# Kernel tuning notes

Hardware: AMD Instinct MI355X
Metric: run time of the kernel (lower is better)

The kernel has to match this reference:

```python
import jax, jax.numpy as jnp
import numpy as np

DIM = 1024
HEADS = 16
HEAD_DIM = DIM // HEADS  # 64
WIN = 256
B, N = 4, 4096


def setup_inputs() -> dict:
    key = jax.random.key(0)
    k1, k2, k3 = jax.random.split(key, 3)
    x = jax.random.normal(k1, (B, N, DIM), dtype=jnp.float32)
    # torch nn.Linear weights: [out_features, in_features]
    Wqkv = jax.random.normal(k2, (3 * DIM, DIM), dtype=jnp.float32) * (DIM ** -0.5)
    Wproj = jax.random.normal(k3, (DIM, DIM), dtype=jnp.float32) * (DIM ** -0.5)
    return {"x": x, "Wqkv": Wqkv, "Wproj": Wproj}


def reference(x, Wqkv, Wproj):
    Bs, Ns, C = x.shape
    H, hd, W = HEADS, HEAD_DIM, WIN
    # qkv projection -> [3, B, H, N, hd]
    qkv = (x @ Wqkv.T).reshape(Bs, Ns, 3, H, hd).transpose(2, 0, 3, 1, 4)
    q, k, v = qkv[0], qkv[1], qkv[2]
    q = q * (hd ** -0.5)
    pad = (W - Ns % W) % W
    if pad:
        pw = ((0, 0), (0, 0), (0, pad), (0, 0))
        q = jnp.pad(q, pw)
        k = jnp.pad(k, pw)
        v = jnp.pad(v, pw)
    Np = Ns + pad
    Df = (Np * hd) // W  # flattened feature dim per window row
    q = q.reshape(Bs * H, W, Df)
    k = k.reshape(Bs * H, W, Df)
    v = v.reshape(Bs * H, W, Df)
    attn = jax.nn.softmax(jnp.einsum('bwd,bxd->bwx', q, k), axis=-1)  # [B*H, W, W]
    out = jnp.einsum('bwx,bxd->bwd', attn, v)
    out = out.reshape(Bs, H, Np, hd)[:, :, :Ns, :].transpose(0, 2, 1, 3).reshape(Bs, Ns, C)
    return out @ Wproj.T
```

## Files before the change

### kernel.cpp

```cpp
#include <hip/hip_runtime.h>
#include <hip/hip_bf16.h>
#include <stdint.h>


using u16 = unsigned short;
typedef __attribute__((ext_vector_type(4))) float f32x4;
typedef __attribute__((ext_vector_type(8))) short s16x8;

#define MFMA_BF16(a, b, c) __builtin_amdgcn_mfma_f32_16x16x32_bf16((a), (b), (c), 0, 0, 0)

__device__ __forceinline__ u16 f2bf(float f) {
  union { float f; uint32_t u; } v; v.f = f;
  uint32_t r = v.u + 0x7fffu + ((v.u >> 16) & 1u);
  return (u16)(r >> 16);
}

__device__ __forceinline__ void gld16(const void* g, void* l) {
  auto gp = (const __attribute__((address_space(1))) void*)(uintptr_t)g;
  auto lp = (__attribute__((address_space(3))) void*)(uint32_t)(uintptr_t)l;
  __builtin_amdgcn_global_load_lds(gp, lp, 16, 0, 0);
}

__global__ __launch_bounds__(256) void cvt_bf16(const float* __restrict__ in,
                                                u16* __restrict__ out, int n8) {
  for (int i = blockIdx.x * blockDim.x + threadIdx.x; i < n8;
       i += gridDim.x * blockDim.x) {
    const float4* p = (const float4*)in + (size_t)i * 2;
    float4 a = p[0], b = p[1];
    s16x8 r;
    r[0] = (short)f2bf(a.x); r[1] = (short)f2bf(a.y);
    r[2] = (short)f2bf(a.z); r[3] = (short)f2bf(a.w);
    r[4] = (short)f2bf(b.x); r[5] = (short)f2bf(b.y);
    r[6] = (short)f2bf(b.z); r[7] = (short)f2bf(b.w);
    *(s16x8*)(out + (size_t)i * 8) = r;
  }
}

template <bool QS, bool F32OUT>
__global__ __launch_bounds__(256) void gemm_bt(const u16* __restrict__ A,
                                               const u16* __restrict__ W,
                                               void* __restrict__ C, int N) {
  __shared__ alignas(16) u16 lA[128 * 32];
  __shared__ alignas(16) u16 lB[128 * 32];
  const int tid = threadIdx.x;
  const int wv = tid >> 6, lane = tid & 63;
  const int fr = lane & 15, fg = lane >> 4;
  const int li = lane >> 2, lc = lane & 3;
  const int bm = blockIdx.x, bn = blockIdx.y;
  const int wm = wv >> 1, wn = wv & 1;

  const f32x4 fz = {0.f, 0.f, 0.f, 0.f};
  f32x4 acc[4][4];
#pragma unroll
  for (int i = 0; i < 4; ++i)
#pragma unroll
    for (int j = 0; j < 4; ++j) acc[i][j] = fz;

  const u16* Ab = A + (size_t)bm * 128 * 1024 + (size_t)lc * 8;
  const u16* Wb = W + (size_t)bn * 128 * 1024 + (size_t)lc * 8;

  for (int kt = 0; kt < 32; ++kt) {
    const int k0 = kt * 32;
#pragma unroll
    for (int j = 0; j < 2; ++j) {
      const int q = wv * 2 + j;
      gld16(Ab + (size_t)(q * 16 + li) * 1024 + k0, lA + q * 512);
      gld16(Wb + (size_t)(q * 16 + li) * 1024 + k0, lB + q * 512);
    }
    __syncthreads();
    s16x8 af[4], bfv[4];
#pragma unroll
    for (int mi = 0; mi < 4; ++mi)
      af[mi] = *(const s16x8*)(lA + (wm * 64 + mi * 16 + fr) * 32 + fg * 8);
#pragma unroll
    for (int ni = 0; ni < 4; ++ni)
      bfv[ni] = *(const s16x8*)(lB + (wn * 64 + ni * 16 + fr) * 32 + fg * 8);
#pragma unroll
    for (int ni = 0; ni < 4; ++ni)
#pragma unroll
      for (int mi = 0; mi < 4; ++mi)
        acc[mi][ni] = MFMA_BF16(af[mi], bfv[ni], acc[mi][ni]);
    __syncthreads();
  }

  const float scale = (QS && bn < 8) ? 0.125f : 1.0f;
#pragma unroll
  for (int mi = 0; mi < 4; ++mi)
#pragma unroll
    for (int ni = 0; ni < 4; ++ni) {
      const int row = bm * 128 + wm * 64 + mi * 16 + fg * 4;
      const int col = bn * 128 + wn * 64 + ni * 16 + fr;
      if (F32OUT) {
        float* cp = (float*)C + (size_t)row * N + col;
#pragma unroll
        for (int r = 0; r < 4; ++r) cp[(size_t)r * N] = acc[mi][ni][r] * scale;
      } else {
        u16* cp = (u16*)C + (size_t)row * N + col;
#pragma unroll
        for (int r = 0; r < 4; ++r) cp[(size_t)r * N] = f2bf(acc[mi][ni][r] * scale);
      }
    }
}

__global__ __launch_bounds__(256) void attn_win(const u16* __restrict__ qkv,
                                                u16* __restrict__ attn) {
  const int bid = blockIdx.x;
  const int bh = (bid & 7) + ((bid >> 5) << 3);
  const int qb = (bid >> 3) & 3;
  const int b = bh >> 4, h = bh & 15;

  const int tid = threadIdx.x;
  const int wv = tid >> 6, lane = tid & 63;
  const int fr = lane & 15, fg = lane >> 4;
  const int li = lane >> 2, lc = lane & 3;

  __shared__ alignas(16) char smem[33792 + 20480];
  u16* lP = (u16*)smem;
  u16* lQ = (u16*)(smem + 33792);
  u16* lK = (u16*)(smem + 33792 + 4096);
  float* redm = (float*)(smem + 33792);
  float* reds = (float*)(smem + 33792 + 1024);
  u16* lVt = (u16*)(smem + 33792);

  const size_t qbase = (size_t)b * 4096 * 3072;

  const f32x4 fz = {0.f, 0.f, 0.f, 0.f};
  f32x4 acc[4][4];
#pragma unroll
  for (int i = 0; i < 4; ++i)
#pragma unroll
    for (int j = 0; j < 4; ++j) acc[i][j] = fz;

  for (int kt = 0; kt < 32; ++kt) {
    const size_t dofs = (size_t)(kt >> 1) * 3072 + h * 64 + (kt & 1) * 32 + lc * 8;
    {
      const int r = wv * 16 + li;
      gld16(qkv + qbase + (size_t)((qb * 64 + r) * 16) * 3072 + dofs, lQ + wv * 512);
    }
#pragma unroll
    for (int j = 0; j < 4; ++j) {
      const int q = wv * 4 + j;
      const int r = q * 16 + li;
      gld16(qkv + qbase + (size_t)(r * 16) * 3072 + 1024 + dofs, lK + q * 512);
    }
    __syncthreads();
    s16x8 qa[4];
#pragma unroll
    for (int mi = 0; mi < 4; ++mi)
      qa[mi] = *(const s16x8*)(lQ + (mi * 16 + fr) * 32 + fg * 8);
#pragma unroll
    for (int ni = 0; ni < 4; ++ni) {
      s16x8 kb = *(const s16x8*)(lK + (wv * 64 + ni * 16 + fr) * 32 + fg * 8);
#pragma unroll
      for (int mi = 0; mi < 4; ++mi)
        acc[mi][ni] = MFMA_BF16(qa[mi], kb, acc[mi][ni]);
    }
    __syncthreads();
  }

  float rmax[4][4], rnrm[4][4];
#pragma unroll
  for (int mi = 0; mi < 4; ++mi)
#pragma unroll
    for (int r = 0; r < 4; ++r) {
      float m = fmaxf(fmaxf(acc[mi][0][r], acc[mi][1][r]),
                      fmaxf(acc[mi][2][r], acc[mi][3][r]));
      for (int o = 1; o < 16; o <<= 1) m = fmaxf(m, __shfl_xor(m, o));
      rmax[mi][r] = m;
    }
  if (fr == 0) {
#pragma unroll
    for (int mi = 0; mi < 4; ++mi)
#pragma unroll
      for (int r = 0; r < 4; ++r) redm[wv * 64 + mi * 16 + fg * 4 + r] = rmax[mi][r];
  }
  __syncthreads();
#pragma unroll
  for (int mi = 0; mi < 4; ++mi)
#pragma unroll
    for (int r = 0; r < 4; ++r) {
      const int row = mi * 16 + fg * 4 + r;
      rmax[mi][r] = fmaxf(fmaxf(redm[row], redm[64 + row]),
                          fmaxf(redm[128 + row], redm[192 + row]));
    }
#pragma unroll
  for (int mi = 0; mi < 4; ++mi)
#pragma unroll
    for (int r = 0; r < 4; ++r) {
      float s = 0.f;
#pragma unroll
      for (int ni = 0; ni < 4; ++ni) {
        float p = exp2f((acc[mi][ni][r] - rmax[mi][r]) * 1.4426950408889634f);
        acc[mi][ni][r] = p;
        s += p;
      }
      for (int o = 1; o < 16; o <<= 1) s += __shfl_xor(s, o);
      rnrm[mi][r] = s;
    }
  if (fr == 0) {
#pragma unroll
    for (int mi = 0; mi < 4; ++mi)
#pragma unroll
      for (int r = 0; r < 4; ++r) reds[wv * 64 + mi * 16 + fg * 4 + r] = rnrm[mi][r];
  }
  __syncthreads();
#pragma unroll
  for (int mi = 0; mi < 4; ++mi)
#pragma unroll
    for (int r = 0; r < 4; ++r) {
      const int row = mi * 16 + fg * 4 + r;
      rnrm[mi][r] = 1.f / (reds[row] + reds[64 + row] + reds[128 + row] + reds[192 + row]);
    }
#pragma unroll
  for (int mi = 0; mi < 4; ++mi)
#pragma unroll
    for (int ni = 0; ni < 4; ++ni)
#pragma unroll
      for (int r = 0; r < 4; ++r)
        lP[(mi * 16 + fg * 4 + r) * 264 + wv * 64 + ni * 16 + fr] =
            f2bf(acc[mi][ni][r] * rnrm[mi][r]);
  __syncthreads();

#pragma unroll 1
  for (int nc = 0; nc < 4; ++nc) {
    f32x4 oacc[4][4];
#pragma unroll
    for (int i = 0; i < 4; ++i)
#pragma unroll
      for (int j = 0; j < 4; ++j) oacc[i][j] = fz;
#pragma unroll 1
    for (int xt = 0; xt < 8; ++xt) {
#pragma unroll
      for (int it = 0; it < 4; ++it) {
        const int id = it * 256 + tid;
        const int xl = id & 31, ng = id >> 5;
        const int d = nc * 256 + ng * 8;
        const u16* g = qkv + qbase +
                       (size_t)((xt * 32 + xl) * 16 + (d >> 6)) * 3072 + 2048 +
                       h * 64 + (d & 63);
        s16x8 v = *(const s16x8*)g;
#pragma unroll
        for (int i = 0; i < 8; ++i) lVt[(ng * 8 + i) * 40 + xl] = (u16)v[i];
      }
      __syncthreads();
      s16x8 pa[4];
#pragma unroll
      for (int mi = 0; mi < 4; ++mi)
        pa[mi] = *(const s16x8*)(lP + (mi * 16 + fr) * 264 + xt * 32 + fg * 8);
#pragma unroll
      for (int ni = 0; ni < 4; ++ni) {
        s16x8 vb = *(const s16x8*)(lVt + (wv * 64 + ni * 16 + fr) * 40 + fg * 8);
#pragma unroll
        for (int mi = 0; mi < 4; ++mi)
          oacc[mi][ni] = MFMA_BF16(pa[mi], vb, oacc[mi][ni]);
      }
      __syncthreads();
    }
#pragma unroll
    for (int mi = 0; mi < 4; ++mi)
#pragma unroll
      for (int ni = 0; ni < 4; ++ni) {
        const int row = mi * 16 + fg * 4;
        const int d = nc * 256 + wv * 64 + ni * 16 + fr;
        const int p = d >> 6, e = d & 63;
        const size_t base =
            (size_t)(b * 4096 + (qb * 64 + row) * 16 + p) * 1024 + h * 64 + e;
#pragma unroll
        for (int r = 0; r < 4; ++r)
          attn[base + (size_t)r * 16 * 1024] = f2bf(oacc[mi][ni][r]);
      }
  }
}

extern "C" void kernel_launch(void* const* d_in, const int* in_sizes, int n_in,
                              void* d_out, int out_size, void* d_ws, size_t ws_size,
                              hipStream_t stream) {
  (void)in_sizes; (void)n_in; (void)out_size; (void)ws_size;
  const float* x = (const float*)d_in[0];
  const float* wqkv = (const float*)d_in[1];
  const float* wproj = (const float*)d_in[2];
  float* out = (float*)d_out;

  char* ws = (char*)d_ws;
  u16* qkv = (u16*)ws;
  u16* xbf = (u16*)(ws + 100663296);
  u16* attn = xbf;
  u16* wqkvb = (u16*)(ws + 134217728);
  u16* wprojb = (u16*)(ws + 140509184);

  cvt_bf16<<<2048, 256, 0, stream>>>(x, xbf, 16777216 / 8);
  cvt_bf16<<<1536, 256, 0, stream>>>(wqkv, wqkvb, 3145728 / 8);
  cvt_bf16<<<512, 256, 0, stream>>>(wproj, wprojb, 1048576 / 8);

  gemm_bt<true, false><<<dim3(128, 24), 256, 0, stream>>>(xbf, wqkvb, qkv, 3072);
  attn_win<<<256, 256, 0, stream>>>(qkv, attn);
  gemm_bt<false, true><<<dim3(128, 8), 256, 0, stream>>>(attn, wprojb, out, 1024);
}
```

Before: 273.2 us.

## Rewrite GEMMs with 256x256 tiles, triple-buffered LDS pipeline and swizzled layout

```diff
diff --git a/kernel.cpp b/kernel.cpp
--- a/kernel.cpp
+++ b/kernel.cpp
@@ -36,60 +36,103 @@
   }
 }
 
-template <bool QS, bool F32OUT>
-__global__ __launch_bounds__(256) void gemm_bt(const u16* __restrict__ A,
-                                               const u16* __restrict__ W,
-                                               void* __restrict__ C, int N) {
-  __shared__ alignas(16) u16 lA[128 * 32];
-  __shared__ alignas(16) u16 lB[128 * 32];
+template <bool QS, bool F32OUT, int GN>
+__global__ __launch_bounds__(512, 2) void gemm256(const u16* __restrict__ A,
+                                                  const u16* __restrict__ W,
+                                                  void* __restrict__ C) {
+  __shared__ alignas(16) u16 lds[3 * 16384];
   const int tid = threadIdx.x;
   const int wv = tid >> 6, lane = tid & 63;
   const int fr = lane & 15, fg = lane >> 4;
-  const int li = lane >> 2, lc = lane & 3;
-  const int bm = blockIdx.x, bn = blockIdx.y;
-  const int wm = wv >> 1, wn = wv & 1;
+  const int wm = wv >> 2, wn = wv & 3;
+  const int N = GN * 256;
+
+  const int nwg = 64 * GN;
+  const int p = blockIdx.x;
+  const int logical = (p & 7) * (nwg >> 3) + (p >> 3);
+  const int bm = logical / GN, bn = logical % GN;
+
+  const int srow = tid >> 2;
+  const int skg = (tid & 3) ^ ((tid >> 3) & 3);
+
+  const u16* As = A + (size_t)(bm * 256 + srow) * 1024 + skg * 8;
+  const u16* Ws = W + (size_t)(bn * 256 + srow) * 1024 + skg * 8;
 
   const f32x4 fz = {0.f, 0.f, 0.f, 0.f};
-  f32x4 acc[4][4];
-#pragma unroll
-  for (int i = 0; i < 4; ++i)
+  f32x4 acc[8][4];
+#pragma unroll
+  for (int i = 0; i < 8; ++i)
 #pragma unroll
     for (int j = 0; j < 4; ++j) acc[i][j] = fz;
 
-  const u16* Ab = A + (size_t)bm * 128 * 1024 + (size_t)lc * 8;
-  const u16* Wb = W + (size_t)bn * 128 * 1024 + (size_t)lc * 8;
-
-  for (int kt = 0; kt < 32; ++kt) {
-    const int k0 = kt * 32;
-#pragma unroll
-    for (int j = 0; j < 2; ++j) {
-      const int q = wv * 2 + j;
-      gld16(Ab + (size_t)(q * 16 + li) * 1024 + k0, lA + q * 512);
-      gld16(Wb + (size_t)(q * 16 + li) * 1024 + k0, lB + q * 512);
-    }
-    __syncthreads();
-    s16x8 af[4], bfv[4];
-#pragma unroll
-    for (int mi = 0; mi < 4; ++mi)
-      af[mi] = *(const s16x8*)(lA + (wm * 64 + mi * 16 + fr) * 32 + fg * 8);
+  auto STAGE = [&](int t) {
+    u16* dst = lds + (t % 3) * 16384;
+    const int k0 = t * 32;
+    gld16(As + k0,              dst + wv * 512);
+    gld16(As + 131072 + k0,     dst + 4096 + wv * 512);
+    gld16(Ws + k0,              dst + 8192 + wv * 512);
+    gld16(Ws + 131072 + k0,     dst + 12288 + wv * 512);
+  };
+
+  STAGE(0);
+  STAGE(1);
+
+  const int rsw = (fg ^ ((fr >> 1) & 3)) * 8;
+  const int aoff = (wm * 128 + fr) * 32 + rsw;
+  const int boff = 8192 + (wn * 64 + fr) * 32 + rsw;
+
+  for (int t = 0; t < 32; ++t) {
+    if (t < 30) {
+      STAGE(t + 2);
+      asm volatile("s_waitcnt vmcnt(8)" ::: "memory");
+    } else if (t == 30) {
+      asm volatile("s_waitcnt vmcnt(4)" ::: "memory");
+    } else {
+      asm volatile("s_waitcnt vmcnt(0)" ::: "memory");
+    }
+    __builtin_amdgcn_s_barrier();
+
+    const u16* buf = lds + (t % 3) * 16384;
+    s16x8 af[8], bfv[4];
+#pragma unroll
+    for (int mi = 0; mi < 4; ++mi)
+      af[mi] = *(const s16x8*)(buf + aoff + mi * 512);
 #pragma unroll
     for (int ni = 0; ni < 4; ++ni)
-      bfv[ni] = *(const s16x8*)(lB + (wn * 64 + ni * 16 + fr) * 32 + fg * 8);
+      bfv[ni] = *(const s16x8*)(buf + boff + ni * 512);
+#pragma unroll
+    for (int mi = 4; mi < 8; ++mi)
+      af[mi] = *(const s16x8*)(buf + aoff + mi * 512);
+
+    asm volatile("s_waitcnt lgkmcnt(4)" ::: "memory");
+    __builtin_amdgcn_sched_barrier(0);
+    __builtin_amdgcn_s_setprio(1);
 #pragma unroll
     for (int ni = 0; ni < 4; ++ni)
 #pragma unroll
       for (int mi = 0; mi < 4; ++mi)
         acc[mi][ni] = MFMA_BF16(af[mi], bfv[ni], acc[mi][ni]);
-    __syncthreads();
-  }
-
-  const float scale = (QS && bn < 8) ? 0.125f : 1.0f;
-#pragma unroll
-  for (int mi = 0; mi < 4; ++mi)
+    __builtin_amdgcn_s_setprio(0);
+
+    asm volatile("s_waitcnt lgkmcnt(0)" ::: "memory");
+    __builtin_amdgcn_sched_barrier(0);
+    __builtin_amdgcn_s_setprio(1);
+#pragma unroll
+    for (int ni = 0; ni < 4; ++ni)
+#pragma unroll
+      for (int mi = 4; mi < 8; ++mi)
+        acc[mi][ni] = MFMA_BF16(af[mi], bfv[ni], acc[mi][ni]);
+    __builtin_amdgcn_s_setprio(0);
+    __builtin_amdgcn_s_barrier();
+  }
+
+  const float scale = (QS && bn < 4) ? 0.125f : 1.0f;
+#pragma unroll
+  for (int mi = 0; mi < 8; ++mi)
 #pragma unroll
     for (int ni = 0; ni < 4; ++ni) {
-      const int row = bm * 128 + wm * 64 + mi * 16 + fg * 4;
-      const int col = bn * 128 + wn * 64 + ni * 16 + fr;
+      const int row = bm * 256 + wm * 128 + mi * 16 + fg * 4;
+      const int col = bn * 256 + wn * 64 + ni * 16 + fr;
       if (F32OUT) {
         float* cp = (float*)C + (size_t)row * N + col;
 #pragma unroll
@@ -292,7 +335,7 @@
   cvt_bf16<<<1536, 256, 0, stream>>>(wqkv, wqkvb, 3145728 / 8);
   cvt_bf16<<<512, 256, 0, stream>>>(wproj, wprojb, 1048576 / 8);
 
-  gemm_bt<true, false><<<dim3(128, 24), 256, 0, stream>>>(xbf, wqkvb, qkv, 3072);
+  gemm256<true, false, 12><<<768, 512, 0, stream>>>(xbf, wqkvb, qkv);
   attn_win<<<256, 256, 0, stream>>>(qkv, attn);
-  gemm_bt<false, true><<<dim3(128, 8), 256, 0, stream>>>(attn, wprojb, out, 1024);
-}
+  gemm256<false, true, 4><<<256, 512, 0, stream>>>(attn, wprojb, out);
+}
```

Result: faster. 245.4 us (-10.2%).
